# Kernel optimization log

Measured on AMD Instinct MI355X. Metric: run time of the kernel, lower is better.

The kernel has to match this reference:

```python
import jax, jax.numpy as jnp
import numpy as np

DIM = 1024
NUM_HEADS = 16
HEAD_DIM = DIM // NUM_HEADS


def setup_inputs() -> dict:
    key = jax.random.key(0)
    ks = jax.random.split(key, 5)
    scale = 1.0 / np.sqrt(DIM)
    return {
        "x": jax.random.normal(ks[0], (2, 2048, DIM), dtype=jnp.float32),
        "qkv_w": jax.random.normal(ks[1], (3 * DIM, DIM), dtype=jnp.float32) * scale,
        "qkv_b": jax.random.normal(ks[2], (3 * DIM,), dtype=jnp.float32) * 0.01,
        "proj_w": jax.random.normal(ks[3], (DIM, DIM), dtype=jnp.float32) * scale,
        "proj_b": jax.random.normal(ks[4], (DIM,), dtype=jnp.float32) * 0.01,
    }


def reference(x, qkv_w, qkv_b, proj_w, proj_b):
    B, N, D = x.shape
    H, Hd = NUM_HEADS, HEAD_DIM
    # fused QKV projection: [B,N,3D]
    qkv = jnp.einsum('bnd,ed->bne', x, qkv_w) + qkv_b
    qkv = qkv.reshape(B, N, 3, H, Hd)
    q = qkv[:, :, 0].transpose(0, 2, 1, 3)  # [B,H,N,Hd]
    k = qkv[:, :, 1].transpose(0, 2, 1, 3)
    v = qkv[:, :, 2].transpose(0, 2, 1, 3)
    scale = 1.0 / jnp.sqrt(jnp.asarray(Hd, dtype=x.dtype))
    scores = jnp.einsum('bhqd,bhkd->bhqk', q, k) * scale  # [B,H,N,N]
    attn = jax.nn.softmax(scores, axis=-1)
    out = jnp.einsum('bhqk,bhkd->bhqd', attn, v)  # [B,H,N,Hd]
    out = out.transpose(0, 2, 1, 3).reshape(B, N, D)
    return jnp.einsum('bnd,ed->bne', out, proj_w) + proj_b
```

## Files before the change

### kernel.cpp

```cpp
#include <hip/hip_runtime.h>
#include <hip/hip_bf16.h>
#include <stdint.h>


typedef __bf16 bf16;
typedef __bf16 bf16x4 __attribute__((ext_vector_type(4)));
typedef __bf16 bf16x8 __attribute__((ext_vector_type(8)));
typedef float  f32x4  __attribute__((ext_vector_type(4)));
typedef float  f32x16 __attribute__((ext_vector_type(16)));
typedef uint32_t u32x4 __attribute__((ext_vector_type(4)));

#define QSCALE 0.18033688011112042f

__device__ __forceinline__ void gload_lds16(const void* g, void* l) {
    __builtin_amdgcn_global_load_lds(
        (const __attribute__((address_space(1))) void*)(uintptr_t)g,
        (__attribute__((address_space(3))) void*)(uint32_t)(uintptr_t)l,
        16, 0, 0);
}

__device__ __forceinline__ uint32_t pkbf(float a, float b) {
    uint16_t lo = __builtin_bit_cast(uint16_t, (bf16)a);
    uint16_t hi = __builtin_bit_cast(uint16_t, (bf16)b);
    return (uint32_t)lo | ((uint32_t)hi << 16);
}

__global__ void cast_all(const float* __restrict__ x,
                         const float* __restrict__ qw,
                         const float* __restrict__ pw,
                         bf16* __restrict__ xb, bf16* __restrict__ wq,
                         bf16* __restrict__ wp) {
    int i = blockIdx.x * blockDim.x + threadIdx.x;
    const float4* src; bf16x4* dst; int off;
    if (i < 1048576)      { src = (const float4*)x;  dst = (bf16x4*)xb; off = i; }
    else if (i < 1835008) { src = (const float4*)qw; dst = (bf16x4*)wq; off = i - 1048576; }
    else                  { src = (const float4*)pw; dst = (bf16x4*)wp; off = i - 1835008; }
    float4 v = src[off];
    bf16x4 o = { (bf16)v.x, (bf16)v.y, (bf16)v.z, (bf16)v.w };
    dst[off] = o;
}

template<int EPI>
__global__ __launch_bounds__(256) void gemm128(
    const bf16* __restrict__ A,
    const bf16* __restrict__ Bw,
    const float* __restrict__ bias,
    float* __restrict__ outF,
    bf16* __restrict__ qb, bf16* __restrict__ kf, bf16* __restrict__ vf,
    int K)
{
    __shared__ bf16 As[128 * 32];
    __shared__ bf16 Bs[128 * 32];
    __shared__ bf16 ct[EPI == 0 ? 128 * 144 : 1];
    const int tid  = threadIdx.x;
    const int lane = tid & 63, w = tid >> 6;
    const int g = lane >> 4, lr = lane & 15;
    const int wr = w >> 1, wc = w & 1;
    const int mbase = blockIdx.y * 128, nbase = blockIdx.x * 128;

    f32x4 acc[4][4] = {};

    const bf16* Ag = A  + (size_t)mbase * K;
    const bf16* Bg = Bw + (size_t)nbase * K;

    for (int kt = 0; kt < K; kt += 32) {
        {
            int c0 = tid;
            gload_lds16(Ag + (size_t)(c0 >> 2) * K + (c0 & 3) * 8, As + c0 * 8);
            gload_lds16(Bg + (size_t)(c0 >> 2) * K + (c0 & 3) * 8, Bs + c0 * 8);
            int c1 = 256 + tid;
            gload_lds16(Ag + (size_t)(c1 >> 2) * K + (c1 & 3) * 8, As + c1 * 8);
            gload_lds16(Bg + (size_t)(c1 >> 2) * K + (c1 & 3) * 8, Bs + c1 * 8);
        }
        __syncthreads();
        bf16x8 af[4], bfr[4];
        #pragma unroll
        for (int mi = 0; mi < 4; ++mi)
            af[mi] = *(const bf16x8*)(As + (wr * 64 + mi * 16 + lr) * 32 + g * 8);
        #pragma unroll
        for (int ni = 0; ni < 4; ++ni)
            bfr[ni] = *(const bf16x8*)(Bs + (wc * 64 + ni * 16 + lr) * 32 + g * 8);
        #pragma unroll
        for (int mi = 0; mi < 4; ++mi)
            #pragma unroll
            for (int ni = 0; ni < 4; ++ni)
                acc[mi][ni] = __builtin_amdgcn_mfma_f32_16x16x32_bf16(
                    af[mi], bfr[ni], acc[mi][ni], 0, 0, 0);
        __syncthreads();
        Ag += 32; Bg += 32;
    }

    if (EPI == 1) {
        #pragma unroll
        for (int ni = 0; ni < 4; ++ni) {
            int e = nbase + wc * 64 + ni * 16 + lr;
            float bv = bias[e];
            #pragma unroll
            for (int mi = 0; mi < 4; ++mi) {
                #pragma unroll
                for (int r = 0; r < 4; ++r) {
                    int token = mbase + wr * 64 + mi * 16 + g * 4 + r;
                    outF[(size_t)token * 1024 + e] = acc[mi][ni][r] + bv;
                }
            }
        }
    } else {
        const int sec = nbase >> 10;
        #pragma unroll
        for (int ni = 0; ni < 4; ++ni) {
            int ec = wc * 64 + ni * 16 + lr;
            float bv = bias[nbase + ec];
            #pragma unroll
            for (int mi = 0; mi < 4; ++mi) {
                #pragma unroll
                for (int r = 0; r < 4; ++r) {
                    int tl = wr * 64 + mi * 16 + g * 4 + r;
                    float v = acc[mi][ni][r] + bv;
                    if (sec == 0) v *= QSCALE;
                    int row = (sec == 2) ? ec : tl;
                    int col = (sec == 2) ? tl : ec;
                    ct[row * 144 + col] = (bf16)v;
                }
            }
        }
        __syncthreads();
        const int b  = mbase >> 11;
        const int h0 = (nbase & 1023) >> 6;
        const int mb = mbase & 2047;
        #pragma unroll
        for (int si = 0; si < 8; ++si) {
            int c   = si * 256 + tid;
            int hh  = c >> 10;
            int w10 = c & 1023;
            int bh  = b * 16 + h0 + hh;
            int lrow, lcol;
            size_t gaddr;
            bf16* dst;
            if (sec == 0) {
                int nl = w10 >> 3, d0 = (w10 & 7) * 8;
                lrow = nl; lcol = hh * 64 + d0;
                gaddr = ((size_t)bh * 2048 + mb + nl) * 64 + d0;
                dst = qb;
            } else if (sec == 1) {
                int o = w10 * 8;
                int frag = o >> 9, l = (o >> 3) & 63;
                int nl = (frag >> 2) * 32 + (l & 31);
                int d0 = (frag & 3) * 16 + (l >> 5) * 8;
                lrow = nl; lcol = hh * 64 + d0;
                gaddr = ((size_t)(bh * 64 + (mb >> 5))) * 2048 + o;
                dst = kf;
            } else {
                int o = w10 * 8;
                int n6 = o >> 12, r2 = o & 4095;
                int d5 = r2 >> 11, r3 = r2 & 2047;
                int nc = r3 >> 9,  l  = (r3 >> 3) & 63;
                int d  = d5 * 32 + (l & 31);
                int n0 = n6 * 64 + nc * 16 + (l >> 5) * 8;
                lrow = hh * 64 + d; lcol = n0;
                gaddr = ((size_t)(bh * 32 + (mb >> 6))) * 4096 + o;
                dst = vf;
            }
            *(bf16x8*)(dst + gaddr) = *(const bf16x8*)(&ct[lrow * 144 + lcol]);
        }
    }
}

__global__ __launch_bounds__(512, 4) void attn32(
    const bf16* __restrict__ Q,
    const bf16* __restrict__ Kf,
    const bf16* __restrict__ Vf,
    bf16* __restrict__ Ao,
    int Nseq)
{
    __shared__ __align__(16) char smem[65536];
    bf16*  KsB = (bf16*)smem;
    bf16*  VsB = (bf16*)(smem + 32768);
    float* xch = (float*)smem;
    bf16*  otp = (bf16*)(smem + 36864);

    const int tid  = threadIdx.x;
    const int lane = tid & 63;
    const int u    = tid >> 6;
    const int half = u >> 2, qw = u & 3;
    const int hi = lane >> 5, ql = lane & 31;
    const int bid = blockIdx.x;
    const int xcd = bid & 7, ii = bid >> 3;
    const int bh = xcd * 4 + (ii >> 4), qc = ii & 15;
    const int h = bh & 15, b = bh >> 4;
    const int q0 = qc * 128 + qw * 32;

    const bf16* Qh  = Q  + (size_t)bh * Nseq * 64;
    const bf16* Kfh = Kf + (size_t)bh * Nseq * 64;
    const bf16* Vfh = Vf + (size_t)bh * Nseq * 64;

    bf16x8 qf[4];
    #pragma unroll
    for (int c = 0; c < 4; ++c)
        qf[c] = *(const bf16x8*)(Qh + (size_t)(q0 + ql) * 64 + c * 16 + hi * 8);

    f32x16 o0 = {}, o1 = {};
    f32x16 lv = {};

    const int nch = (Nseq >> 6) >> 1;
    const int hk  = half * nch;

    auto stage = [&](int buf, int t) {
        const bf16* Kc = Kfh + (size_t)(hk + t) * 4096;
        const bf16* Vc = Vfh + (size_t)(hk + t) * 4096;
        bf16* kd = KsB + (half * 2 + buf) * 4096;
        bf16* vd = VsB + (half * 2 + buf) * 4096;
        int ht = tid & 255;
        gload_lds16(Kc + ht * 8,        kd + ht * 8);
        gload_lds16(Kc + 2048 + ht * 8, kd + 2048 + ht * 8);
        gload_lds16(Vc + ht * 8,        vd + ht * 8);
        gload_lds16(Vc + 2048 + ht * 8, vd + 2048 + ht * 8);
    };

    stage(0, 0);
    __syncthreads();

    for (int t = 0; t < nch; ++t) {
        const int cur = t & 1;
        if (t + 1 < nch) stage(cur ^ 1, t + 1);

        const bf16* kl = KsB + (half * 2 + cur) * 4096;
        const bf16* vl = VsB + (half * 2 + cur) * 4096;
        bf16x8 kin[8], vfr[8];
        #pragma unroll
        for (int i = 0; i < 8; ++i)
            kin[i] = *(const bf16x8*)(kl + i * 512 + lane * 8);
        #pragma unroll
        for (int i = 0; i < 8; ++i)
            vfr[i] = *(const bf16x8*)(vl + i * 512 + lane * 8);

        f32x16 s0 = {}, s1 = {};
        #pragma unroll
        for (int c = 0; c < 4; ++c) {
            s0 = __builtin_amdgcn_mfma_f32_32x32x16_bf16(kin[c],     qf[c], s0, 0, 0, 0);
            s1 = __builtin_amdgcn_mfma_f32_32x32x16_bf16(kin[4 + c], qf[c], s1, 0, 0, 0);
        }

        float p0[16], p1[16];
        #pragma unroll
        for (int r = 0; r < 16; ++r) { p0[r] = __builtin_amdgcn_exp2f(s0[r]); }
        #pragma unroll
        for (int r = 0; r < 16; ++r) { p1[r] = __builtin_amdgcn_exp2f(s1[r]); }
        #pragma unroll
        for (int r = 0; r < 16; ++r) { lv[r] += p0[r] + p1[r]; }

        bf16x8 pfr[4];
        #pragma unroll
        for (int f = 0; f < 4; ++f) {
            const float* pp = (f < 2) ? p0 : p1;
            const int base = (f & 1) * 8;
            union { uint32_t u[4]; bf16x8 v; } pw;
            #pragma unroll
            for (int wd = 0; wd < 2; ++wd) {
                uint32_t X = pkbf(pp[base + 2*wd], pp[base + 2*wd + 1]);
                uint32_t Y = pkbf(pp[base + 4 + 2*wd], pp[base + 4 + 2*wd + 1]);
                auto rr = __builtin_amdgcn_permlane32_swap((int)X, (int)Y, false, false);
                pw.u[wd]     = (uint32_t)rr[0];
                pw.u[2 + wd] = (uint32_t)rr[1];
            }
            pfr[f] = pw.v;
        }

        #pragma unroll
        for (int f = 0; f < 4; ++f) {
            o0 = __builtin_amdgcn_mfma_f32_32x32x16_bf16(vfr[f],     pfr[f], o0, 0, 0, 0);
            o1 = __builtin_amdgcn_mfma_f32_32x32x16_bf16(vfr[4 + f], pfr[f], o1, 0, 0, 0);
        }

        __syncthreads();
    }

    float lsum = lv[0];
    #pragma unroll
    for (int r = 1; r < 16; ++r) lsum += lv[r];
    lsum += __shfl_xor(lsum, 32);

    if (half == 1) {
        float* xp = xch + ((size_t)(qw * 64 + lane)) * 36;
        *(f32x16*)(xp)      = o0;
        *(f32x16*)(xp + 16) = o1;
        xp[32] = lsum;
    }
    __syncthreads();
    if (half == 0) {
        const float* xp = xch + ((size_t)(qw * 64 + lane)) * 36;
        f32x16 oa = *(const f32x16*)(xp);
        f32x16 ob = *(const f32x16*)(xp + 16);
        o0 += oa; o1 += ob; lsum += xp[32];

        float linv = __builtin_amdgcn_rcpf(lsum);

        #pragma unroll
        for (int qd = 0; qd < 4; ++qd) {
            int dbase = 8 * qd + 4 * hi;
            bf16* orow = otp + (qw * 32 + ql) * 66;
            *(uint32_t*)(orow + dbase)          = pkbf(o0[4*qd] * linv,   o0[4*qd+1] * linv);
            *(uint32_t*)(orow + dbase + 2)      = pkbf(o0[4*qd+2] * linv, o0[4*qd+3] * linv);
            *(uint32_t*)(orow + 32 + dbase)     = pkbf(o1[4*qd] * linv,   o1[4*qd+1] * linv);
            *(uint32_t*)(orow + 32 + dbase + 2) = pkbf(o1[4*qd+2] * linv, o1[4*qd+3] * linv);
        }
        __asm__ volatile("s_waitcnt lgkmcnt(0)" ::: "memory");
        const int t = lane >> 1, e = lane & 1;
        uint32_t rw[16];
        #pragma unroll
        for (int j = 0; j < 16; ++j)
            rw[j] = *(const uint32_t*)(otp + (qw * 32 + t) * 66 + e * 32 + 2 * j);
        size_t gbase = (size_t)(b * Nseq + q0 + t) * 1024 + h * 64 + e * 32;
        #pragma unroll
        for (int v = 0; v < 4; ++v) {
            u32x4 sv = { rw[4*v], rw[4*v+1], rw[4*v+2], rw[4*v+3] };
            *(u32x4*)(Ao + gbase + v * 8) = sv;
        }
    }
}

extern "C" void kernel_launch(void* const* d_in, const int* in_sizes, int n_in,
                              void* d_out, int out_size, void* d_ws, size_t ws_size,
                              hipStream_t stream) {
    const float* x      = (const float*)d_in[0];
    const float* qkv_w  = (const float*)d_in[1];
    const float* qkv_b  = (const float*)d_in[2];
    const float* proj_w = (const float*)d_in[3];
    const float* proj_b = (const float*)d_in[4];
    float* out = (float*)d_out;

    char* ws = (char*)d_ws;
    bf16* xb    = (bf16*)(ws);
    bf16* wqkv  = (bf16*)(ws + ((size_t)8  << 20));
    bf16* wproj = (bf16*)(ws + ((size_t)14 << 20));
    bf16* qb    = (bf16*)(ws + ((size_t)16 << 20));
    bf16* kf    = (bf16*)(ws + ((size_t)24 << 20));
    bf16* vf    = (bf16*)(ws + ((size_t)32 << 20));
    bf16* att   = (bf16*)(ws);

    cast_all<<<dim3(8192), dim3(256), 0, stream>>>(x, qkv_w, proj_w, xb, wqkv, wproj);

    gemm128<0><<<dim3(24, 32), dim3(256), 0, stream>>>(
        xb, wqkv, qkv_b, (float*)nullptr, qb, kf, vf, 1024);

    attn32<<<dim3(512), dim3(512), 0, stream>>>(qb, kf, vf, att, 2048);

    gemm128<1><<<dim3(8, 32), dim3(256), 0, stream>>>(
        att, wproj, proj_b, out, (bf16*)nullptr, (bf16*)nullptr, (bf16*)nullptr, 1024);
}
```

Measured before the change: 121.6 us.

## Double-buffer GEMM LDS tiles and alias epilogue buffer onto staging memory

The GEMM main loop now uses two LDS stage buffers: the next K-slice is issued with global_load_lds before computing on the current one, so global-to-LDS traffic can overlap the MFMA work and one barrier per iteration is removed. The staging buffers and the EPI==0 epilogue transpose buffer now share one raw shared array. That lowers LDS use for the QKV GEMM and may allow more resident blocks. The overlap depends on how the barrier waits for the asynchronous LDS loads, and reusing the buffer relies on the final loop barrier before the epilogue.

```diff
diff --git a/kernel.cpp b/kernel.cpp
--- a/kernel.cpp
+++ b/kernel.cpp
@@ -49,9 +49,8 @@
     bf16* __restrict__ qb, bf16* __restrict__ kf, bf16* __restrict__ vf,
     int K)
 {
-    __shared__ bf16 As[128 * 32];
-    __shared__ bf16 Bs[128 * 32];
-    __shared__ bf16 ct[EPI == 0 ? 128 * 144 : 1];
+    __shared__ __align__(16) char gsm[EPI == 0 ? 36864 : 32768];
+    bf16* ct = (bf16*)gsm;
     const int tid  = threadIdx.x;
     const int lane = tid & 63, w = tid >> 6;
     const int g = lane >> 4, lr = lane & 15;
@@ -60,34 +59,43 @@
 
     f32x4 acc[4][4] = {};
 
-    const bf16* Ag = A  + (size_t)mbase * K;
-    const bf16* Bg = Bw + (size_t)nbase * K;
-
-    for (int kt = 0; kt < K; kt += 32) {
-        {
-            int c0 = tid;
-            gload_lds16(Ag + (size_t)(c0 >> 2) * K + (c0 & 3) * 8, As + c0 * 8);
-            gload_lds16(Bg + (size_t)(c0 >> 2) * K + (c0 & 3) * 8, Bs + c0 * 8);
-            int c1 = 256 + tid;
-            gload_lds16(Ag + (size_t)(c1 >> 2) * K + (c1 & 3) * 8, As + c1 * 8);
-            gload_lds16(Bg + (size_t)(c1 >> 2) * K + (c1 & 3) * 8, Bs + c1 * 8);
-        }
-        __syncthreads();
+    auto stg = [&](int buf, int it) {
+        const bf16* Ag = A  + (size_t)mbase * K + it * 32;
+        const bf16* Bg = Bw + (size_t)nbase * K + it * 32;
+        bf16* as = (bf16*)(gsm + buf * 16384);
+        bf16* bs = (bf16*)(gsm + buf * 16384 + 8192);
+        int c0 = tid, c1 = 256 + tid;
+        gload_lds16(Ag + (size_t)(c0 >> 2) * K + (c0 & 3) * 8, as + c0 * 8);
+        gload_lds16(Bg + (size_t)(c0 >> 2) * K + (c0 & 3) * 8, bs + c0 * 8);
+        gload_lds16(Ag + (size_t)(c1 >> 2) * K + (c1 & 3) * 8, as + c1 * 8);
+        gload_lds16(Bg + (size_t)(c1 >> 2) * K + (c1 & 3) * 8, bs + c1 * 8);
+    };
+
+    const int nIt = K >> 5;
+    stg(0, 0);
+    __syncthreads();
+
+    for (int it = 0; it < nIt; ++it) {
+        const int cur = it & 1;
+        if (it + 1 < nIt) stg(cur ^ 1, it + 1);
+
+        const bf16* as = (const bf16*)(gsm + cur * 16384);
+        const bf16* bs = as + 4096;
         bf16x8 af[4], bfr[4];
         #pragma unroll
         for (int mi = 0; mi < 4; ++mi)
-            af[mi] = *(const bf16x8*)(As + (wr * 64 + mi * 16 + lr) * 32 + g * 8);
+            af[mi] = *(const bf16x8*)(as + (wr * 64 + mi * 16 + lr) * 32 + g * 8);
         #pragma unroll
         for (int ni = 0; ni < 4; ++ni)
-            bfr[ni] = *(const bf16x8*)(Bs + (wc * 64 + ni * 16 + lr) * 32 + g * 8);
+            bfr[ni] = *(const bf16x8*)(bs + (wc * 64 + ni * 16 + lr) * 32 + g * 8);
         #pragma unroll
         for (int mi = 0; mi < 4; ++mi)
             #pragma unroll
             for (int ni = 0; ni < 4; ++ni)
                 acc[mi][ni] = __builtin_amdgcn_mfma_f32_16x16x32_bf16(
                     af[mi], bfr[ni], acc[mi][ni], 0, 0, 0);
+
         __syncthreads();
-        Ag += 32; Bg += 32;
     }
 
     if (EPI == 1) {
```

Result: faster. 112.6 us (-7.4%).
